# Optimization experiments

Measured on AMD Instinct MI355X. Metric: run time of the kernel, lower is better.

Reference implementation:

```python
import jax, jax.numpy as jnp
import numpy as np

N_FFT = 512
HOP = N_FFT // 4  # torch.stft default hop_length
SR = 16000
SS = 340.4
DIST = 1.0


def _hann(n):
    # torch.hann_window default is periodic
    return (0.5 * (1.0 - jnp.cos(2.0 * jnp.pi * jnp.arange(n) / n))).astype(jnp.float32)


def _stft(x):
    # x: [N, L] -> complex [N, F, T]; matches torch.stft(center=True, pad_mode='reflect', onesided=True)
    pad = N_FFT // 2
    xp = jnp.pad(x, ((0, 0), (pad, pad)), mode='reflect')
    T = (xp.shape[1] - N_FFT) // HOP + 1
    idx = jnp.arange(T)[:, None] * HOP + jnp.arange(N_FFT)[None, :]  # [T, n_fft]
    frames = xp[:, idx] * _hann(N_FFT)[None, None, :]                # [N, T, n_fft]
    X = jnp.fft.rfft(frames, axis=-1)                                # [N, T, F]
    return jnp.swapaxes(X, 1, 2)                                     # [N, F, T]


def setup_inputs() -> dict:
    key = jax.random.key(0)
    k1, k2, k3 = jax.random.split(key, 3)
    B, C, L = 16, 4, 160000
    x = jax.random.normal(k1, (B, C, L), dtype=jnp.float32)
    angle = jax.random.uniform(k2, (B, 1), dtype=jnp.float32) * 360.0
    mic_pos = jax.random.normal(k3, (B, C, 3), dtype=jnp.float32) * 0.05
    return {"x": x, "angle": angle, "mic_pos": mic_pos}


def reference(x, angle, mic_pos):
    B, C, L = x.shape
    X = _stft(x.reshape(B * C, L))            # [B*C, F, T] complex
    Fdim, T = X.shape[1], X.shape[2]
    X = X.reshape(B, C, Fdim, T)

    # 'X' feature: real/imag concat over channel dim -> [B, 2C, F, T]
    featX = jnp.concatenate([X.real, X.imag], axis=1)

    # 'SV' feature: steering vectors
    ang = angle[:, 0]
    half_pi = jnp.float32(np.pi / 2)
    sin90 = jnp.sin(half_pi)
    cos90 = jnp.cos(half_pi)  # ~0, kept for faithfulness
    rad = -ang * (jnp.pi / 180.0)
    loc_src = jnp.stack([
        DIST * jnp.cos(rad) * sin90,
        DIST * jnp.sin(rad) * sin90,
        jnp.full_like(ang, DIST * cos90),
    ], axis=1)  # [B, 3]

    # Original computes torch.norm over the FULL [B,3] difference per mic i (a scalar),
    # so TDOA is identical across batch: Frobenius norm over (B, 3) axes.
    TDOA = jnp.sqrt(jnp.sum((mic_pos - loc_src[:, None, :]) ** 2, axis=(0, 2)))  # [C]
    TDOA = TDOA - TDOA[0]
    TDOA = jnp.broadcast_to(TDOA[None, :], (B, C))  # [B, C]

    # Steering[b,c,f] = exp(f * TDOA[b,c] * const), const = -1j*2*pi*sr/(n_fft*ss)
    coef = -2.0 * jnp.pi * SR / (N_FFT * SS)
    phase = coef * jnp.arange(Fdim, dtype=jnp.float32)[None, None, :] * TDOA[:, :, None]  # [B,C,F]
    sv = jnp.exp(1j * phase)  # complex64, unit magnitude
    sv = sv / jnp.linalg.norm(sv, axis=1, keepdims=True)  # normalize over channels
    sv = jnp.broadcast_to(sv[..., None], (B, C, Fdim, T))
    featSV = jnp.concatenate([sv.real, sv.imag], axis=1)  # [B, 2C, F, T]

    feature = jnp.concatenate([featX, featSV], axis=1)    # [B, 4C, F, T]
    feature = feature.reshape(B, 4 * C * Fdim, T)
    return jnp.transpose(feature, (0, 2, 1))               # [B, T, 4C*F]
```

## Files before the change

### kernel.cpp

```cpp
#include <hip/hip_runtime.h>
#include <math.h>

#define L_SIG 160000
#define HOPC 128
#define FD 257
#define TDIM 1251
#define ROW 4112
#define NROWS (16 * TDIM)
#define NBC 64
#define NFR (NBC * TDIM)
#define NPAIR (NFR / 2)

typedef float floatx4 __attribute__((ext_vector_type(4)));


__global__ __launch_bounds__(256) void setup_kernel(const float* __restrict__ angle,
                                                    const float* __restrict__ mic,
                                                    float* __restrict__ tbl) {
    int tid = threadIdx.x;
    __shared__ float tdoa[4];
    if (tid == 0) {
        const float half_pi = (float)(M_PI / 2.0);
        float s90 = sinf(half_pi);
        float c90 = cosf(half_pi);
        float acc0 = 0.f, acc1 = 0.f, acc2 = 0.f, acc3 = 0.f;
        for (int b = 0; b < 16; ++b) {
            float ang = angle[b];
            float rad = -ang * (float)(M_PI / 180.0);
            float lx = cosf(rad) * s90;
            float ly = sinf(rad) * s90;
            float lz = c90;
            #pragma unroll
            for (int c = 0; c < 4; ++c) {
                const float* m = mic + ((size_t)b * 4 + c) * 3;
                float dx = m[0] - lx, dy = m[1] - ly, dz = m[2] - lz;
                float s = dx * dx + dy * dy + dz * dz;
                if (c == 0) acc0 += s; else if (c == 1) acc1 += s;
                else if (c == 2) acc2 += s; else acc3 += s;
            }
        }
        float t0 = sqrtf(acc0);
        tdoa[0] = 0.0f;
        tdoa[1] = sqrtf(acc1) - t0;
        tdoa[2] = sqrtf(acc2) - t0;
        tdoa[3] = sqrtf(acc3) - t0;
    }
    __syncthreads();
    const float coef = (float)(-2.0 * M_PI * 16000.0 / (512.0 * 340.4));
    for (int i = tid; i < 4 * FD; i += 256) {
        int c = i / FD;
        int f = i - c * FD;
        float ph = coef * (float)f * tdoa[c];
        tbl[i]        = cosf(ph) * 0.5f;
        tbl[1028 + i] = sinf(ph) * 0.5f;
    }
}

__global__ __launch_bounds__(512) void sv_bcast(const float* __restrict__ tbl,
                                                float* __restrict__ out) {
    const int row = blockIdx.x;
    const int tid = threadIdx.x;
    const floatx4* S4 = (const floatx4*)tbl;
    floatx4* dst = (floatx4*)(out + (size_t)row * ROW + 2056);
    floatx4 v0 = S4[tid];
    __builtin_nontemporal_store(v0, dst + tid);
    if (tid < 2) {
        floatx4 v1 = S4[512 + tid];
        __builtin_nontemporal_store(v1, dst + 512 + tid);
    }
}

__device__ __forceinline__ void bfly8(float (&zr)[8], float (&zi)[8]) {
    const float C = 0.70710678118654752440f;
    float sr0=zr[0]+zr[4], si0=zi[0]+zi[4], dr0=zr[0]-zr[4], di0=zi[0]-zi[4];
    float sr1=zr[1]+zr[5], si1=zi[1]+zi[5], dr1=zr[1]-zr[5], di1=zi[1]-zi[5];
    float sr2=zr[2]+zr[6], si2=zi[2]+zi[6], dr2=zr[2]-zr[6], di2=zi[2]-zi[6];
    float sr3=zr[3]+zr[7], si3=zi[3]+zi[7], dr3=zr[3]-zr[7], di3=zi[3]-zi[7];
    float t;
    t = C*(dr1+di1); di1 = C*(di1-dr1); dr1 = t;
    t = dr2; dr2 = di2; di2 = -t;
    t = C*(di3-dr3); di3 = -C*(dr3+di3); dr3 = t;
    float p0r=sr0+sr2, p0i=si0+si2, p1r=sr1+sr3, p1i=si1+si3;
    float q0r=sr0-sr2, q0i=si0-si2, q1r=sr1-sr3, q1i=si1-si3;
    zr[0]=p0r+p1r; zi[0]=p0i+p1i;
    zr[2]=q0r+q1i; zi[2]=q0i-q1r;
    zr[4]=p0r-p1r; zi[4]=p0i-p1i;
    zr[6]=q0r-q1i; zi[6]=q0i+q1r;
    p0r=dr0+dr2; p0i=di0+di2; p1r=dr1+dr3; p1i=di1+di3;
    q0r=dr0-dr2; q0i=di0-di2; q1r=dr1-dr3; q1i=di1-di3;
    zr[1]=p0r+p1r; zi[1]=p0i+p1i;
    zr[3]=q0r+q1i; zi[3]=q0i-q1r;
    zr[5]=p0r-p1r; zi[5]=p0i-p1i;
    zr[7]=q0r-q1i; zi[7]=q0i+q1r;
}

__device__ __forceinline__ void cmul(float& r, float& i, float ar, float ai, float br, float bi) {
    r = ar * br - ai * bi;
    i = ar * bi + ai * br;
}

__device__ __forceinline__ void twiddle8(float (&zr)[8], float (&zi)[8], float wr, float wi) {
    float p2r, p2i, p3r, p3i, p4r, p4i, p5r, p5i, p6r, p6i, p7r, p7i;
    cmul(p2r, p2i, wr, wi, wr, wi);
    cmul(p3r, p3i, p2r, p2i, wr, wi);
    cmul(p4r, p4i, p2r, p2i, p2r, p2i);
    cmul(p5r, p5i, p4r, p4i, wr, wi);
    cmul(p6r, p6i, p3r, p3i, p3r, p3i);
    cmul(p7r, p7i, p4r, p4i, p3r, p3i);
    float t;
    t = zr[1]*wr - zi[1]*wi;  zi[1] = zr[1]*wi + zi[1]*wr;  zr[1] = t;
    t = zr[2]*p2r - zi[2]*p2i; zi[2] = zr[2]*p2i + zi[2]*p2r; zr[2] = t;
    t = zr[3]*p3r - zi[3]*p3i; zi[3] = zr[3]*p3i + zi[3]*p3r; zr[3] = t;
    t = zr[4]*p4r - zi[4]*p4i; zi[4] = zr[4]*p4i + zi[4]*p4r; zr[4] = t;
    t = zr[5]*p5r - zi[5]*p5i; zi[5] = zr[5]*p5i + zi[5]*p5r; zr[5] = t;
    t = zr[6]*p6r - zi[6]*p6i; zi[6] = zr[6]*p6i + zi[6]*p6r; zr[6] = t;
    t = zr[7]*p7r - zi[7]*p7i; zi[7] = zr[7]*p7i + zi[7]*p7r; zr[7] = t;
}

#define PHYS(i) ((i) + ((i) >> 3))

__global__ __launch_bounds__(256) void stft8_kernel(const float* __restrict__ x,
                                                    float* __restrict__ out) {
    __shared__ float2 exch[4][576];
    const int tid = threadIdx.x;
    const int wv  = tid >> 6;
    const int j   = tid & 63;
    const int pid = blockIdx.x * 4 + wv;
    const int fid0 = 2 * pid;
    const int fid1 = fid0 + 1;
    const int t0 = fid0 % TDIM, bc0 = fid0 / TDIM;
    const int t1 = fid1 % TDIM, bc1 = fid1 / TDIM;

    const float PI_256 = 0.012271846303085129838f;
    float sj, cj;
    __sincosf((float)j * PI_256, &sj, &cj);
    const float R2 = 0.70710678118654752440f;
    float cv[8];
    cv[0] = cj;            cv[1] = (cj - sj) * R2;
    cv[2] = -sj;           cv[3] = (-cj - sj) * R2;
    cv[4] = -cj;           cv[5] = (sj - cj) * R2;
    cv[6] = sj;            cv[7] = (cj + sj) * R2;

    const float* xs0 = x + (size_t)bc0 * L_SIG;
    const float* xs1 = x + (size_t)bc1 * L_SIG;
    const int g0 = t0 * HOPC - 256 + j;
    const int g1 = t1 * HOPC - 256 + j;
    float zr[8], zi[8];
    #pragma unroll
    for (int r = 0; r < 8; ++r) {
        int a0 = g0 + 64 * r; a0 = (a0 < 0) ? -a0 : a0; if (a0 >= L_SIG) a0 = 2 * L_SIG - 2 - a0;
        int a1 = g1 + 64 * r; a1 = (a1 < 0) ? -a1 : a1; if (a1 >= L_SIG) a1 = 2 * L_SIG - 2 - a1;
        float w = 0.5f - 0.5f * cv[r];
        zr[r] = xs0[a0] * w;
        zi[r] = xs1[a1] * w;
    }

    float2* buf = exch[wv];

    bfly8(zr, zi);
    twiddle8(zr, zi, cj, -sj);
    #pragma unroll
    for (int k = 0; k < 8; ++k) {
        int idx = 8 * j + k;
        buf[PHYS(idx)] = make_float2(zr[k], zi[k]);
    }
    #pragma unroll
    for (int r = 0; r < 8; ++r) {
        int idx = j + 64 * r;
        float2 v = buf[PHYS(idx)];
        zr[r] = v.x; zi[r] = v.y;
    }

    bfly8(zr, zi);
    float s1v, c1v;
    __sincosf((float)(j & ~7) * PI_256, &s1v, &c1v);
    twiddle8(zr, zi, c1v, -s1v);
    #pragma unroll
    for (int k = 0; k < 8; ++k) {
        int idx = 64 * (j >> 3) + (j & 7) + 8 * k;
        buf[PHYS(idx)] = make_float2(zr[k], zi[k]);
    }
    #pragma unroll
    for (int r = 0; r < 8; ++r) {
        int idx = j + 64 * r;
        float2 v = buf[PHYS(idx)];
        zr[r] = v.x; zi[r] = v.y;
    }

    bfly8(zr, zi);

    const int srcl = (64 - j) & 63;
    float pr_[8], pi_[8];
    #pragma unroll
    for (int m = 0; m < 8; ++m) {
        pr_[m] = __shfl(zr[m], srcl, 64);
        pi_[m] = __shfl(zi[m], srcl, 64);
    }

    const int b0 = bc0 >> 2, c0 = bc0 & 3;
    const int b1 = bc1 >> 2, c1 = bc1 & 3;
    const size_t base0 = ((size_t)b0 * TDIM + t0) * ROW + (size_t)c0 * FD;
    const size_t base1 = ((size_t)b1 * TDIM + t1) * ROW + (size_t)c1 * FD;
    const bool l0 = (j == 0);

    #pragma unroll
    for (int k = 0; k < 5; ++k) {
        float Pr = l0 ? pr_[(8 - k) & 7] : pr_[7 - k];
        float Pi = l0 ? pi_[(8 - k) & 7] : pi_[7 - k];
        float F0r = 0.5f * (zr[k] + Pr);
        float F0i = 0.5f * (zi[k] - Pi);
        float F1r = 0.5f * (zi[k] + Pi);
        float F1i = 0.5f * (Pr - zr[k]);
        int f = j + 64 * k;
        if (k < 4 || l0) {
            __builtin_nontemporal_store(F0r, out + base0 + f);
            __builtin_nontemporal_store(F0i, out + base0 + 1028 + f);
            __builtin_nontemporal_store(F1r, out + base1 + f);
            __builtin_nontemporal_store(F1i, out + base1 + 1028 + f);
        }
    }
}

extern "C" void kernel_launch(void* const* d_in, const int* in_sizes, int n_in,
                              void* d_out, int out_size, void* d_ws, size_t ws_size,
                              hipStream_t stream) {
    const float* x     = (const float*)d_in[0];
    const float* angle = (const float*)d_in[1];
    const float* mic   = (const float*)d_in[2];
    float* out = (float*)d_out;
    float* tbl = (float*)d_ws;

    setup_kernel<<<1, 256, 0, stream>>>(angle, mic, tbl);
    stft8_kernel<<<NPAIR / 4, 256, 0, stream>>>(x, out);
    sv_bcast<<<NROWS, 512, 0, stream>>>(tbl, out);
}
```

Baseline: 455.0 us.

## Fuse steering-vector broadcast into STFT kernel and skip reflect math for interior frames

Removes the separate sv_bcast kernel launch and instead has each STFT wave whose channel is 0 write the steering-vector half of its output row. This saves one kernel launch and its tail, and lets the SV stores overlap with FFT work. It also adds a fast path that skips reflect-padding index arithmetic when both frames lie in the interior. The cost is extra store work and divergence concentrated on the channel-0 waves, which unbalances the load across waves.

```diff
diff --git a/kernel.cpp b/kernel.cpp
--- a/kernel.cpp
+++ b/kernel.cpp
@@ -56,20 +56,6 @@
     }
 }
 
-__global__ __launch_bounds__(512) void sv_bcast(const float* __restrict__ tbl,
-                                                float* __restrict__ out) {
-    const int row = blockIdx.x;
-    const int tid = threadIdx.x;
-    const floatx4* S4 = (const floatx4*)tbl;
-    floatx4* dst = (floatx4*)(out + (size_t)row * ROW + 2056);
-    floatx4 v0 = S4[tid];
-    __builtin_nontemporal_store(v0, dst + tid);
-    if (tid < 2) {
-        floatx4 v1 = S4[512 + tid];
-        __builtin_nontemporal_store(v1, dst + 512 + tid);
-    }
-}
-
 __device__ __forceinline__ void bfly8(float (&zr)[8], float (&zi)[8]) {
     const float C = 0.70710678118654752440f;
     float sr0=zr[0]+zr[4], si0=zi[0]+zi[4], dr0=zr[0]-zr[4], di0=zi[0]-zi[4];
@@ -120,6 +106,7 @@
 #define PHYS(i) ((i) + ((i) >> 3))
 
 __global__ __launch_bounds__(256) void stft8_kernel(const float* __restrict__ x,
+                                                    const float* __restrict__ tbl,
                                                     float* __restrict__ out) {
     __shared__ float2 exch[4][576];
     const int tid = threadIdx.x;
@@ -146,13 +133,25 @@
     const int g0 = t0 * HOPC - 256 + j;
     const int g1 = t1 * HOPC - 256 + j;
     float zr[8], zi[8];
-    #pragma unroll
-    for (int r = 0; r < 8; ++r) {
-        int a0 = g0 + 64 * r; a0 = (a0 < 0) ? -a0 : a0; if (a0 >= L_SIG) a0 = 2 * L_SIG - 2 - a0;
-        int a1 = g1 + 64 * r; a1 = (a1 < 0) ? -a1 : a1; if (a1 >= L_SIG) a1 = 2 * L_SIG - 2 - a1;
-        float w = 0.5f - 0.5f * cv[r];
-        zr[r] = xs0[a0] * w;
-        zi[r] = xs1[a1] * w;
+
+    const bool in0 = (t0 >= 2) && (t0 < 1249);
+    const bool in1 = (t1 >= 2) && (t1 < 1249);
+    if (in0 && in1) {
+        #pragma unroll
+        for (int r = 0; r < 8; ++r) {
+            float w = 0.5f - 0.5f * cv[r];
+            zr[r] = xs0[g0 + 64 * r] * w;
+            zi[r] = xs1[g1 + 64 * r] * w;
+        }
+    } else {
+        #pragma unroll
+        for (int r = 0; r < 8; ++r) {
+            int a0 = g0 + 64 * r; a0 = (a0 < 0) ? -a0 : a0; if (a0 >= L_SIG) a0 = 2 * L_SIG - 2 - a0;
+            int a1 = g1 + 64 * r; a1 = (a1 < 0) ? -a1 : a1; if (a1 >= L_SIG) a1 = 2 * L_SIG - 2 - a1;
+            float w = 0.5f - 0.5f * cv[r];
+            zr[r] = xs0[a0] * w;
+            zi[r] = xs1[a1] * w;
+        }
     }
 
     float2* buf = exch[wv];
@@ -219,6 +218,28 @@
             __builtin_nontemporal_store(F1i, out + base1 + 1028 + f);
         }
     }
+
+    const floatx4* S4 = (const floatx4*)tbl;
+    if (c0 == 0) {
+        floatx4* dst = (floatx4*)(out + base0 + 2056);
+        #pragma unroll
+        for (int it = 0; it < 8; ++it) {
+            int i4 = 64 * it + j;
+            __builtin_nontemporal_store(S4[i4], dst + i4);
+        }
+        if (j < 2)
+            __builtin_nontemporal_store(S4[512 + j], dst + 512 + j);
+    }
+    if (c1 == 0) {
+        floatx4* dst = (floatx4*)(out + base1 + 2056);
+        #pragma unroll
+        for (int it = 0; it < 8; ++it) {
+            int i4 = 64 * it + j;
+            __builtin_nontemporal_store(S4[i4], dst + i4);
+        }
+        if (j < 2)
+            __builtin_nontemporal_store(S4[512 + j], dst + 512 + j);
+    }
 }
 
 extern "C" void kernel_launch(void* const* d_in, const int* in_sizes, int n_in,
@@ -231,6 +252,5 @@
     float* tbl = (float*)d_ws;
 
     setup_kernel<<<1, 256, 0, stream>>>(angle, mic, tbl);
-    stft8_kernel<<<NPAIR / 4, 256, 0, stream>>>(x, out);
-    sv_bcast<<<NROWS, 512, 0, stream>>>(tbl, out);
-}
+    stft8_kernel<<<NPAIR / 4, 256, 0, stream>>>(x, tbl, out);
+}
```

Result: faster. 430.0 us (-5.5%).
